# Optimization experiments

Hardware: AMD Instinct MI355X
Metric: run time of the kernel (lower is better)

The kernel has to match this reference:

```python
import jax, jax.numpy as jnp
import numpy as np

N_NODES = 50000
N_EDGES = 300000
D = 256  # node/edge feature dim; MLP input = 3*D = 768


def setup_inputs() -> dict:
    key = jax.random.key(0)
    ks = jax.random.split(key, 5)
    x_node = jax.random.normal(ks[0], (N_NODES, D), dtype=jnp.float32)
    x_edge = jax.random.normal(ks[1], (N_EDGES, D), dtype=jnp.float32)
    edge_index = jax.random.randint(ks[2], (2, N_EDGES), 0, N_NODES, dtype=jnp.int64)
    # MLP params: Linear(3*D, D) -> ReLU -> Linear(D, D)
    W1 = jax.random.normal(ks[3], (3 * D, D), dtype=jnp.float32) * (1.0 / np.sqrt(3 * D))
    b1 = jnp.zeros((D,), dtype=jnp.float32)
    W2 = jax.random.normal(ks[4], (D, D), dtype=jnp.float32) * (1.0 / np.sqrt(D))
    b2 = jnp.zeros((D,), dtype=jnp.float32)
    return {"x_node": x_node, "x_edge": x_edge, "edge_index": edge_index,
            "W1": W1, "b1": b1, "W2": W2, "b2": b2}


def reference(x_node, x_edge, edge_index, W1, b1, W2, b2):
    # gather src/dst node feats and concat with edge feats: [E, 3*D]
    src = x_node[edge_index[0]]
    dst = x_node[edge_index[1]]
    h = jnp.concatenate([src, dst, x_edge], axis=1)
    # MLP (custom_func): Linear -> ReLU -> Linear
    h = jax.nn.relu(h @ W1 + b1)
    x_edge_ = h @ W2 + b2
    return x_edge_
```

## Files before the change

kernel.cpp:

```cpp
#include <hip/hip_runtime.h>


typedef __attribute__((ext_vector_type(8))) short short8;
typedef __attribute__((ext_vector_type(4))) float f32x4;
typedef __attribute__((address_space(1))) unsigned int* gp1_t;
typedef __attribute__((address_space(3))) unsigned int* lp3_t;

#define WAITV(N) asm volatile("s_waitcnt vmcnt(" #N ")" ::: "memory")
#define WAITL0   asm volatile("s_waitcnt lgkmcnt(0)" ::: "memory")
#define BAR()    __builtin_amdgcn_s_barrier()

#define AS_OFF 0
#define BS_OFF 24576
#define HS_OFF 73728
#define SMEM_SZ 139264
#define LDO 260

__device__ __forceinline__ unsigned short f2b(float f) {
  unsigned int u = __float_as_uint(f);
  return (unsigned short)((u + 0x7FFFu + ((u >> 16) & 1u)) >> 16);
}
__device__ __forceinline__ unsigned int f2b2(float lo, float hi) {
  return (unsigned int)f2b(lo) | ((unsigned int)f2b(hi) << 16);
}
__device__ __forceinline__ void gload16(const void* g, void* l) {
  __builtin_amdgcn_global_load_lds((gp1_t)g, (lp3_t)l, 16, 0, 0);
}

__global__ void prep_w_kernel(const float* __restrict__ w,
                              unsigned short* __restrict__ wp, int total) {
  int i = blockIdx.x * 256 + threadIdx.x;
  if (i >= total) return;
  int kc = i >> 13;
  int rem = i & 8191;
  int n = rem >> 5;
  int s = (rem >> 3) & 3;
  int j = rem & 7;
  int kin = (((s - (n >> 1)) & 3) << 3) | j;
  wp[i] = f2b(w[(size_t)(kc * 32 + kin) * 256 + n]);
}

__global__ void conv_bf16_kernel(const float* __restrict__ x,
                                 unsigned short* __restrict__ y, int n4) {
  int i = blockIdx.x * 256 + threadIdx.x;
  if (i >= n4) return;
  float4 v = ((const float4*)x)[i];
  ushort4 u;
  u.x = f2b(v.x); u.y = f2b(v.y); u.z = f2b(v.z); u.w = f2b(v.w);
  ((ushort4*)y)[i] = u;
}

__global__ __launch_bounds__(512, 2) void edge_mlp_full(
    const float* __restrict__ xedge, const int* __restrict__ eidx,
    const unsigned short* __restrict__ nodeb,
    const unsigned short* __restrict__ wt1p, const float* __restrict__ b1,
    const unsigned short* __restrict__ wt2p, const float* __restrict__ b2,
    float* __restrict__ out, int E) {
  __shared__ __align__(16) char smem[SMEM_SZ];
  char* As = smem + AS_OFF;
  char* Bs = smem + BS_OFF;
  char* Hs = smem + HS_OFF;

  const int t = threadIdx.x, w = t >> 6, l = t & 63;
  const int lr = l & 15, lk = l >> 4;
  const int wr = w >> 2, wc = w & 3;
  const int row4 = t >> 2, c4 = t & 3;
  const int ebase = blockIdx.x * 128;

  int e = ebase + row4;
  if (e >= E) e = E - 1;
  const int isrc = eidx[e], idst = eidx[E + e];
  const int swg = (c4 - (row4 >> 1)) & 3;

  f32x4 acc[4][4];
#pragma unroll
  for (int i = 0; i < 4; ++i)
#pragma unroll
    for (int j = 0; j < 4; ++j) acc[i][j] = (f32x4)0.0f;

  auto stageB = [&](const unsigned short* wp, int c, int buf) {
    const char* g = (const char*)wp + (size_t)c * 16384 + t * 16;
    char* lb = Bs + buf * 16384 + (w << 10);
    gload16(g, lb);
    gload16(g + 8192, lb + 8192);
  };
  auto gloadA = [&](int c, int buf) {
    const int nid = (c < 8) ? isrc : idst;
    const char* g = (const char*)nodeb + (size_t)nid * 512 + (c & 7) * 64 + swg * 16;
    gload16(g, As + buf * 8192 + (w << 10));
  };
  auto edge_issue = [&](int c, float4& a, float4& b) {
    const float* p = xedge + (size_t)e * 256 + (c - 16) * 32 + c4 * 8;
    a = ((const float4*)p)[0];
    b = ((const float4*)p)[1];
  };
  auto edge_write = [&](int c, const float4& a, const float4& b) {
    uint4 u;
    u.x = f2b2(a.x, a.y); u.y = f2b2(a.z, a.w);
    u.z = f2b2(b.x, b.y); u.w = f2b2(b.z, b.w);
    const int sw = (c4 + (row4 >> 1)) & 3;
    *(uint4*)(As + (c % 3) * 8192 + row4 * 64 + sw * 16) = u;
  };
  auto fragsA = [&](int buf, short8 (&af)[4]) {
#pragma unroll
    for (int mi = 0; mi < 4; ++mi) {
      const int row = wr * 64 + mi * 16 + lr;
      const int slot = (lk + (row >> 1)) & 3;
      af[mi] = *(const short8*)(As + buf * 8192 + row * 64 + slot * 16);
    }
  };
  auto fragsB = [&](int buf, short8 (&bf)[4]) {
#pragma unroll
    for (int ni = 0; ni < 4; ++ni) {
      const int row = wc * 64 + ni * 16 + lr;
      const int slot = (lk + (row >> 1)) & 3;
      bf[ni] = *(const short8*)(Bs + buf * 16384 + row * 64 + slot * 16);
    }
  };
  auto domfma = [&](short8 (&af)[4], short8 (&bf)[4]) {
    __builtin_amdgcn_s_setprio(1);
#pragma unroll
    for (int mi = 0; mi < 4; ++mi)
#pragma unroll
      for (int ni = 0; ni < 4; ++ni)
        acc[mi][ni] = __builtin_amdgcn_mfma_f32_16x16x32_bf16(
            af[mi], bf[ni], acc[mi][ni], 0, 0, 0);
    __builtin_amdgcn_s_setprio(0);
  };

  short8 af[4], bf[4];
  float4 eA0, eA1, eB0, eB1;

  stageB(wt1p, 0, 0); gloadA(0, 0);
  stageB(wt1p, 1, 1); gloadA(1, 1);

  for (int k = 0; k < 14; ++k) {
    WAITV(3);
    BAR();
    fragsA(k % 3, af); fragsB(k % 3, bf);
    stageB(wt1p, k + 2, (k + 2) % 3);
    gloadA(k + 2, (k + 2) % 3);
    domfma(af, bf);
  }
  {
    WAITV(3);
    BAR();
    fragsA(2, af); fragsB(2, bf);
    stageB(wt1p, 16, 1);
    edge_issue(16, eA0, eA1);
    domfma(af, bf);
  }
  for (int kk = 15; kk < 23; kk += 2) {
    WAITV(4);
    BAR();
    fragsA(kk % 3, af); fragsB(kk % 3, bf);
    stageB(wt1p, kk + 2, (kk + 2) % 3);
    edge_issue(kk + 2, eB0, eB1);
    domfma(af, bf);
    edge_write(kk + 1, eA0, eA1);
    WAITL0;
    WAITV(4);
    BAR();
    fragsA((kk + 1) % 3, af); fragsB((kk + 1) % 3, bf);
    if (kk + 3 < 24) {
      stageB(wt1p, kk + 3, (kk + 3) % 3);
      edge_issue(kk + 3, eA0, eA1);
    } else {
      stageB(wt2p, 0, 0);
    }
    domfma(af, bf);
    edge_write(kk + 2, eB0, eB1);
    WAITL0;
  }
  {
    WAITV(2);
    BAR();
    fragsA(2, af); fragsB(2, bf);
    stageB(wt2p, 1, 1);
    domfma(af, bf);
  }

#pragma unroll
  for (int ni = 0; ni < 4; ++ni) {
    const int col = wc * 64 + ni * 16 + lr;
    const float bias = b1[col];
    const int cole = col & ~1;
    const int chunk = cole >> 3;
    const int cb = (cole & 6) * 2;
#pragma unroll
    for (int mi = 0; mi < 4; ++mi) {
      float v[4], p[4];
#pragma unroll
      for (int r = 0; r < 4; ++r) {
        float x = acc[mi][ni][r] + bias;
        v[r] = x > 0.f ? x : 0.f;
        acc[mi][ni][r] = 0.f;
      }
#pragma unroll
      for (int r = 0; r < 4; ++r) p[r] = __shfl_xor(v[r], 1, 64);
      const int r0 = (lr & 1) ? 2 : 0;
#pragma unroll
      for (int rr = 0; rr < 2; ++rr) {
        const int r = r0 + rr;
        const int row = wr * 64 + mi * 16 + lk * 4 + r;
        const float lo = (lr & 1) ? p[r] : v[r];
        const float hi = (lr & 1) ? v[r] : p[r];
        *(unsigned int*)(Hs + row * 512 + ((chunk ^ (row & 7)) << 4) + cb) =
            f2b2(lo, hi);
      }
    }
  }
  WAITL0;

#pragma unroll
  for (int u = 0; u < 8; ++u) {
    if (u < 7) { WAITV(2); } else { WAITV(0); }
    BAR();
    short8 af2[4], bf2[4];
#pragma unroll
    for (int mi = 0; mi < 4; ++mi) {
      const int row = wr * 64 + mi * 16 + lr;
      af2[mi] = *(const short8*)(Hs + row * 512 +
                                 ((((u << 2) + lk) ^ (row & 7)) << 4));
    }
    fragsB((24 + u) % 3, bf2);
    if (u < 6) stageB(wt2p, u + 2, (26 + u) % 3);
    domfma(af2, bf2);
  }

  float* outst = (float*)smem;
#pragma unroll
  for (int p = 0; p < 2; ++p) {
    __syncthreads();
    if (wr == p) {
#pragma unroll
      for (int ni = 0; ni < 4; ++ni) {
        const int col = wc * 64 + ni * 16 + lr;
        const float bias = b2[col];
#pragma unroll
        for (int mi = 0; mi < 4; ++mi)
#pragma unroll
          for (int r = 0; r < 4; ++r)
            outst[(mi * 16 + lk * 4 + r) * LDO + col] = acc[mi][ni][r] + bias;
      }
    }
    __syncthreads();
#pragma unroll
    for (int it = 0; it < 8; ++it) {
      const int idx = it * 2048 + t * 4;
      const int lrow = idx >> 8;
      const int cc = idx & 255;
      const int grow = ebase + p * 64 + lrow;
      if (grow < E)
        *(float4*)(out + (size_t)grow * 256 + cc) =
            *(const float4*)(outst + lrow * LDO + cc);
    }
  }
}

__global__ __launch_bounds__(512, 2) void edge_mlp_simple(
    const float* __restrict__ xnode, const float* __restrict__ xedge,
    const int* __restrict__ eidx,
    const unsigned short* __restrict__ wt1p, const float* __restrict__ b1,
    const unsigned short* __restrict__ wt2p, const float* __restrict__ b2,
    float* __restrict__ out, int E) {
  __shared__ __align__(16) char smem[90112];
  char* As = smem;
  char* Bs = smem + 8192;
  char* Hs = smem + 24576;

  const int t = threadIdx.x, w = t >> 6, l = t & 63;
  const int lr = l & 15, lk = l >> 4;
  const int wr = w >> 2, wc = w & 3;
  const int row4 = t >> 2, c4 = t & 3;
  const int ebase = blockIdx.x * 128;
  int e = ebase + row4;
  if (e >= E) e = E - 1;
  const int isrc = eidx[e], idst = eidx[E + e];

  f32x4 acc[4][4];
#pragma unroll
  for (int i = 0; i < 4; ++i)
#pragma unroll
    for (int j = 0; j < 4; ++j) acc[i][j] = (f32x4)0.0f;

  auto stageB1 = [&](const unsigned short* wp, int c) {
    const char* g = (const char*)wp + (size_t)c * 16384 + t * 16;
    char* lb = Bs + (w << 10);
    gload16(g, lb);
    gload16(g + 8192, lb + 8192);
  };
  auto mfma16 = [&](short8 (&af)[4], short8 (&bf)[4]) {
#pragma unroll
    for (int mi = 0; mi < 4; ++mi)
#pragma unroll
      for (int ni = 0; ni < 4; ++ni)
        acc[mi][ni] = __builtin_amdgcn_mfma_f32_16x16x32_bf16(
            af[mi], bf[ni], acc[mi][ni], 0, 0, 0);
  };

  for (int c = 0; c < 24; ++c) {
    stageB1(wt1p, c);
    const float* p = ((c < 8) ? xnode + (size_t)isrc * 256
                              : (c < 16) ? xnode + (size_t)idst * 256
                                         : xedge + (size_t)e * 256) +
                     (c & 7) * 32 + c4 * 8;
    float4 a = ((const float4*)p)[0], b = ((const float4*)p)[1];
    uint4 u;
    u.x = f2b2(a.x, a.y); u.y = f2b2(a.z, a.w);
    u.z = f2b2(b.x, b.y); u.w = f2b2(b.z, b.w);
    const int sw = (c4 + (row4 >> 1)) & 3;
    *(uint4*)(As + row4 * 64 + sw * 16) = u;
    __syncthreads();
    short8 af[4], bf[4];
#pragma unroll
    for (int mi = 0; mi < 4; ++mi) {
      const int row = wr * 64 + mi * 16 + lr;
      const int slot = (lk + (row >> 1)) & 3;
      af[mi] = *(const short8*)(As + row * 64 + slot * 16);
    }
#pragma unroll
    for (int ni = 0; ni < 4; ++ni) {
      const int row = wc * 64 + ni * 16 + lr;
      const int slot = (lk + (row >> 1)) & 3;
      bf[ni] = *(const short8*)(Bs + row * 64 + slot * 16);
    }
    mfma16(af, bf);
    __syncthreads();
  }

#pragma unroll
  for (int ni = 0; ni < 4; ++ni) {
    const int col = wc * 64 + ni * 16 + lr;
    const float bias = b1[col];
#pragma unroll
    for (int mi = 0; mi < 4; ++mi)
#pragma unroll
      for (int r = 0; r < 4; ++r) {
        float x = acc[mi][ni][r] + bias;
        x = x > 0.f ? x : 0.f;
        const int row = wr * 64 + mi * 16 + lk * 4 + r;
        *(unsigned short*)(Hs + row * 512 + ((col >> 3) ^ (row & 7)) * 16 +
                           (col & 7) * 2) = f2b(x);
        acc[mi][ni][r] = 0.f;
      }
  }
  __syncthreads();

  for (int u = 0; u < 8; ++u) {
    stageB1(wt2p, u);
    __syncthreads();
    short8 af[4], bf[4];
#pragma unroll
    for (int mi = 0; mi < 4; ++mi) {
      const int row = wr * 64 + mi * 16 + lr;
      af[mi] = *(const short8*)(Hs + row * 512 +
                                ((((u << 2) + lk) ^ (row & 7)) << 4));
    }
#pragma unroll
    for (int ni = 0; ni < 4; ++ni) {
      const int row = wc * 64 + ni * 16 + lr;
      const int slot = (lk + (row >> 1)) & 3;
      bf[ni] = *(const short8*)(Bs + row * 64 + slot * 16);
    }
    mfma16(af, bf);
    __syncthreads();
  }

  float* outst = (float*)smem;
#pragma unroll
  for (int p = 0; p < 2; ++p) {
    __syncthreads();
    if (wr == p) {
#pragma unroll
      for (int ni = 0; ni < 4; ++ni) {
        const int col = wc * 64 + ni * 16 + lr;
        const float bias = b2[col];
#pragma unroll
        for (int mi = 0; mi < 4; ++mi)
#pragma unroll
          for (int r = 0; r < 4; ++r)
            outst[(mi * 16 + lk * 4 + r) * LDO + col] = acc[mi][ni][r] + bias;
      }
    }
    __syncthreads();
#pragma unroll
    for (int it = 0; it < 8; ++it) {
      const int idx = it * 2048 + t * 4;
      const int lrow = idx >> 8;
      const int cc = idx & 255;
      const int grow = ebase + p * 64 + lrow;
      if (grow < E)
        *(float4*)(out + (size_t)grow * 256 + cc) =
            *(const float4*)(outst + lrow * LDO + cc);
    }
  }
}

extern "C" void kernel_launch(void* const* d_in, const int* in_sizes, int n_in,
                              void* d_out, int out_size, void* d_ws, size_t ws_size,
                              hipStream_t stream) {
  const float* xnode = (const float*)d_in[0];
  const float* xedge = (const float*)d_in[1];
  const int* eidx = (const int*)d_in[2];
  const float* W1 = (const float*)d_in[3];
  const float* b1 = (const float*)d_in[4];
  const float* W2 = (const float*)d_in[5];
  const float* b2 = (const float*)d_in[6];
  float* out = (float*)d_out;

  const int NN = in_sizes[0] / 256;
  const int E = in_sizes[1] / 256;

  char* ws = (char*)d_ws;
  unsigned short* wt1p = (unsigned short*)ws;
  unsigned short* wt2p = (unsigned short*)(ws + 24 * 16384);
  unsigned short* nodeb = (unsigned short*)(ws + 32 * 16384);
  const size_t need_full = (size_t)32 * 16384 + (size_t)NN * 512;

  prep_w_kernel<<<(24 * 8192 + 255) / 256, 256, 0, stream>>>(W1, wt1p, 24 * 8192);
  prep_w_kernel<<<(8 * 8192 + 255) / 256, 256, 0, stream>>>(W2, wt2p, 8 * 8192);

  const int grid = (E + 127) / 128;
  if (ws_size >= need_full) {
    const int n4 = NN * 64;
    conv_bf16_kernel<<<(n4 + 255) / 256, 256, 0, stream>>>(xnode, nodeb, n4);
    edge_mlp_full<<<grid, 512, 0, stream>>>(xedge, eidx, nodeb, wt1p, b1,
                                            wt2p, b2, out, E);
  } else {
    edge_mlp_simple<<<grid, 512, 0, stream>>>(xnode, xedge, eidx, wt1p, b1,
                                              wt2p, b2, out, E);
  }
}
```

Measured before the change: 381.7 us.

## Read weight fragments directly from global memory and shrink LDS to double buffer

```diff
diff --git a/kernel.cpp b/kernel.cpp
--- a/kernel.cpp
+++ b/kernel.cpp
@@ -6,14 +6,7 @@
 typedef __attribute__((address_space(1))) unsigned int* gp1_t;
 typedef __attribute__((address_space(3))) unsigned int* lp3_t;
 
-#define WAITV(N) asm volatile("s_waitcnt vmcnt(" #N ")" ::: "memory")
-#define WAITL0   asm volatile("s_waitcnt lgkmcnt(0)" ::: "memory")
-#define BAR()    __builtin_amdgcn_s_barrier()
-
-#define AS_OFF 0
-#define BS_OFF 24576
-#define HS_OFF 73728
-#define SMEM_SZ 139264
+#define SMEM_SZ 66560
 #define LDO 260
 
 __device__ __forceinline__ unsigned short f2b(float f) {
@@ -50,16 +43,15 @@
   ((ushort4*)y)[i] = u;
 }
 
-__global__ __launch_bounds__(512, 2) void edge_mlp_full(
+__global__ __launch_bounds__(512, 4) void edge_mlp_full(
     const float* __restrict__ xedge, const int* __restrict__ eidx,
     const unsigned short* __restrict__ nodeb,
     const unsigned short* __restrict__ wt1p, const float* __restrict__ b1,
     const unsigned short* __restrict__ wt2p, const float* __restrict__ b2,
     float* __restrict__ out, int E) {
   __shared__ __align__(16) char smem[SMEM_SZ];
-  char* As = smem + AS_OFF;
-  char* Bs = smem + BS_OFF;
-  char* Hs = smem + HS_OFF;
+  char* As = smem;
+  char* Hs = smem;
 
   const int t = threadIdx.x, w = t >> 6, l = t & 63;
   const int lr = l & 15, lk = l >> 4;
@@ -72,52 +64,51 @@
   const int isrc = eidx[e], idst = eidx[E + e];
   const int swg = (c4 - (row4 >> 1)) & 3;
 
+  int aoff[4], boff[4];
+#pragma unroll
+  for (int mi = 0; mi < 4; ++mi) {
+    const int row = wr * 64 + mi * 16 + lr;
+    aoff[mi] = row * 64 + (((lk + (row >> 1)) & 3) << 4);
+  }
+#pragma unroll
+  for (int ni = 0; ni < 4; ++ni) {
+    const int row = wc * 64 + ni * 16 + lr;
+    boff[ni] = row * 64 + (((lk + (row >> 1)) & 3) << 4);
+  }
+
   f32x4 acc[4][4];
 #pragma unroll
   for (int i = 0; i < 4; ++i)
 #pragma unroll
     for (int j = 0; j < 4; ++j) acc[i][j] = (f32x4)0.0f;
 
-  auto stageB = [&](const unsigned short* wp, int c, int buf) {
-    const char* g = (const char*)wp + (size_t)c * 16384 + t * 16;
-    char* lb = Bs + buf * 16384 + (w << 10);
-    gload16(g, lb);
-    gload16(g + 8192, lb + 8192);
-  };
   auto gloadA = [&](int c, int buf) {
     const int nid = (c < 8) ? isrc : idst;
     const char* g = (const char*)nodeb + (size_t)nid * 512 + (c & 7) * 64 + swg * 16;
     gload16(g, As + buf * 8192 + (w << 10));
   };
-  auto edge_issue = [&](int c, float4& a, float4& b) {
-    const float* p = xedge + (size_t)e * 256 + (c - 16) * 32 + c4 * 8;
-    a = ((const float4*)p)[0];
-    b = ((const float4*)p)[1];
-  };
-  auto edge_write = [&](int c, const float4& a, const float4& b) {
-    uint4 u;
-    u.x = f2b2(a.x, a.y); u.y = f2b2(a.z, a.w);
-    u.z = f2b2(b.x, b.y); u.w = f2b2(b.z, b.w);
-    const int sw = (c4 + (row4 >> 1)) & 3;
-    *(uint4*)(As + (c % 3) * 8192 + row4 * 64 + sw * 16) = u;
-  };
-  auto fragsA = [&](int buf, short8 (&af)[4]) {
-#pragma unroll
-    for (int mi = 0; mi < 4; ++mi) {
-      const int row = wr * 64 + mi * 16 + lr;
-      const int slot = (lk + (row >> 1)) & 3;
-      af[mi] = *(const short8*)(As + buf * 8192 + row * 64 + slot * 16);
-    }
-  };
-  auto fragsB = [&](int buf, short8 (&bf)[4]) {
-#pragma unroll
-    for (int ni = 0; ni < 4; ++ni) {
-      const int row = wc * 64 + ni * 16 + lr;
-      const int slot = (lk + (row >> 1)) & 3;
-      bf[ni] = *(const short8*)(Bs + buf * 16384 + row * 64 + slot * 16);
-    }
-  };
-  auto domfma = [&](short8 (&af)[4], short8 (&bf)[4]) {
+
+  gloadA(0, 0);
+  __syncthreads();
+
+  for (int k = 0; k < 24; ++k) {
+    const int buf = k & 1, nb = buf ^ 1;
+    const int c = k + 1;
+    float4 m0, m1;
+    if (c < 16) {
+      gloadA(c, nb);
+    } else if (c < 24) {
+      const float* p = xedge + (size_t)e * 256 + (c - 16) * 32 + c4 * 8;
+      m0 = ((const float4*)p)[0];
+      m1 = ((const float4*)p)[1];
+    }
+    short8 af[4], bf[4];
+    const char* ab = As + buf * 8192;
+    const char* wb = (const char*)wt1p + k * 16384;
+#pragma unroll
+    for (int mi = 0; mi < 4; ++mi) af[mi] = *(const short8*)(ab + aoff[mi]);
+#pragma unroll
+    for (int ni = 0; ni < 4; ++ni) bf[ni] = *(const short8*)(wb + boff[ni]);
     __builtin_amdgcn_s_setprio(1);
 #pragma unroll
     for (int mi = 0; mi < 4; ++mi)
@@ -126,58 +117,14 @@
         acc[mi][ni] = __builtin_amdgcn_mfma_f32_16x16x32_bf16(
             af[mi], bf[ni], acc[mi][ni], 0, 0, 0);
     __builtin_amdgcn_s_setprio(0);
-  };
-
-  short8 af[4], bf[4];
-  float4 eA0, eA1, eB0, eB1;
-
-  stageB(wt1p, 0, 0); gloadA(0, 0);
-  stageB(wt1p, 1, 1); gloadA(1, 1);
-
-  for (int k = 0; k < 14; ++k) {
-    WAITV(3);
-    BAR();
-    fragsA(k % 3, af); fragsB(k % 3, bf);
-    stageB(wt1p, k + 2, (k + 2) % 3);
-    gloadA(k + 2, (k + 2) % 3);
-    domfma(af, bf);
-  }
-  {
-    WAITV(3);
-    BAR();
-    fragsA(2, af); fragsB(2, bf);
-    stageB(wt1p, 16, 1);
-    edge_issue(16, eA0, eA1);
-    domfma(af, bf);
-  }
-  for (int kk = 15; kk < 23; kk += 2) {
-    WAITV(4);
-    BAR();
-    fragsA(kk % 3, af); fragsB(kk % 3, bf);
-    stageB(wt1p, kk + 2, (kk + 2) % 3);
-    edge_issue(kk + 2, eB0, eB1);
-    domfma(af, bf);
-    edge_write(kk + 1, eA0, eA1);
-    WAITL0;
-    WAITV(4);
-    BAR();
-    fragsA((kk + 1) % 3, af); fragsB((kk + 1) % 3, bf);
-    if (kk + 3 < 24) {
-      stageB(wt1p, kk + 3, (kk + 3) % 3);
-      edge_issue(kk + 3, eA0, eA1);
-    } else {
-      stageB(wt2p, 0, 0);
-    }
-    domfma(af, bf);
-    edge_write(kk + 2, eB0, eB1);
-    WAITL0;
-  }
-  {
-    WAITV(2);
-    BAR();
-    fragsA(2, af); fragsB(2, bf);
-    stageB(wt2p, 1, 1);
-    domfma(af, bf);
+    if (c >= 16 && c < 24) {
+      uint4 u;
+      u.x = f2b2(m0.x, m0.y); u.y = f2b2(m0.z, m0.w);
+      u.z = f2b2(m1.x, m1.y); u.w = f2b2(m1.z, m1.w);
+      const int sw = (c4 + (row4 >> 1)) & 3;
+      *(uint4*)(As + nb * 8192 + row4 * 64 + sw * 16) = u;
+    }
+    __syncthreads();
   }
 
 #pragma unroll
@@ -210,22 +157,28 @@
       }
     }
   }
-  WAITL0;
+  __syncthreads();
 
 #pragma unroll
   for (int u = 0; u < 8; ++u) {
-    if (u < 7) { WAITV(2); } else { WAITV(0); }
-    BAR();
     short8 af2[4], bf2[4];
+    const char* wb = (const char*)wt2p + u * 16384;
 #pragma unroll
     for (int mi = 0; mi < 4; ++mi) {
       const int row = wr * 64 + mi * 16 + lr;
       af2[mi] = *(const short8*)(Hs + row * 512 +
                                  ((((u << 2) + lk) ^ (row & 7)) << 4));
     }
-    fragsB((24 + u) % 3, bf2);
-    if (u < 6) stageB(wt2p, u + 2, (26 + u) % 3);
-    domfma(af2, bf2);
+#pragma unroll
+    for (int ni = 0; ni < 4; ++ni) bf2[ni] = *(const short8*)(wb + boff[ni]);
+    __builtin_amdgcn_s_setprio(1);
+#pragma unroll
+    for (int mi = 0; mi < 4; ++mi)
+#pragma unroll
+      for (int ni = 0; ni < 4; ++ni)
+        acc[mi][ni] = __builtin_amdgcn_mfma_f32_16x16x32_bf16(
+            af2[mi], bf2[ni], acc[mi][ni], 0, 0, 0);
+    __builtin_amdgcn_s_setprio(0);
   }
 
   float* outst = (float*)smem;
```

After: 361.4 us. 1.06x faster.
